# Performance work log

Measured on AMD Instinct MI355X. Metric: run time of the kernel, lower is better.

## Reference

```python
import jax, jax.numpy as jnp
import numpy as np
import math

B, T, C, H = 4, 2048, 1024, 4
D = C // H
SCALE = 1.0 / math.sqrt(D)
EPS = 1e-5

def _cln(x, w, b):
    # channel-first LayerNorm over C of (B, C, T)
    mu = jnp.mean(x, axis=1, keepdims=True)
    r = x - mu
    s = jnp.mean(r * r, axis=1, keepdims=True)
    return r / jnp.sqrt(s + EPS) * w + b

def _dwconv(x, w, b=None):
    # depthwise conv1d: x (B, C, T), w (C, 1, 3), stride 1, pad 1
    y = jax.lax.conv_general_dilated(x, w, (1,), [(1, 1)], dimension_numbers=('NCH', 'OIH', 'NCH'), feature_group_count=x.shape[1])
    if b is not None:
        y = y + b[None, :, None]
    return y

def _conv1x1(x, w, b):
    # pointwise conv: x (B, C, T), w (Cout, Cin), b (Cout,)
    return jnp.einsum('oc,bct->bot', w, x) + b[None, :, None]

def _forward(x, mask, norm1_w, norm1_b, qconv_w, kconv_w, vconv_w, qnorm_w, qnorm_b, knorm_w, knorm_b, vnorm_w, vnorm_b, q1_w, q1_b, k1_w, k1_b, v1_w, v1_b, proj_w, proj_b, norm2_w, norm2_b, lin1_w, lin1_b, tc_w, tc_b, lin2_w, lin2_b):
    xc = jnp.swapaxes(x, 1, 2)                      # (B, C, T)
    h = _cln(xc, norm1_w, norm1_b)
    mf = mask.astype(x.dtype)                       # (B, 1, T); stride 1 -> interpolate is identity
    q = _conv1x1(_cln(_dwconv(h, qconv_w) * mf, qnorm_w, qnorm_b), q1_w, q1_b)
    k = _conv1x1(_cln(_dwconv(h, kconv_w) * mf, knorm_w, knorm_b), k1_w, k1_b)
    v = _conv1x1(_cln(_dwconv(h, vconv_w) * mf, vnorm_w, vnorm_b), v1_w, v1_b)
    # (B, H, T, D)
    q = jnp.swapaxes(q.reshape(B, H, D, T), 2, 3)
    k = jnp.swapaxes(k.reshape(B, H, D, T), 2, 3)
    v = jnp.swapaxes(v.reshape(B, H, D, T), 2, 3)
    att = jnp.einsum('bhqd,bhkd->bhqk', q * SCALE, k)
    att = jnp.where(mask[:, :, None, :], att, -jnp.inf)
    att = jax.nn.softmax(att, axis=-1)
    out = jnp.einsum('bhqk,bhkd->bhqd', att, v * mf[:, :, :, None])
    out = jnp.swapaxes(out, 2, 3).reshape(B, C, T)
    out = _conv1x1(out, proj_w, proj_b) * mf        # qx_mask == mask for stride 1
    x = x + jnp.swapaxes(out, 1, 2)                 # residual, (B, T, C)
    # Local_cnn branch
    h2 = jnp.swapaxes(_cln(jnp.swapaxes(x, 1, 2), norm2_w, norm2_b), 1, 2)  # (B, T, C)
    y = h2 @ lin1_w.T + lin1_b
    y = jnp.swapaxes(_dwconv(jnp.swapaxes(y, 1, 2), tc_w, tc_b), 1, 2)
    y = jax.nn.gelu(y, approximate=False)
    y = y @ lin2_w.T + lin2_b
    return x + y

def setup_inputs():
    key = jax.random.key(0)
    ks = jax.random.split(key, 16)
    f32 = jnp.float32
    x = jax.random.normal(ks[0], (B, T, C), dtype=f32)
    lengths = jax.random.randint(ks[1], (B,), T // 2, T + 1)
    mask = jnp.arange(T)[None, None, :] < lengths[:, None, None]  # (B, 1, T) bool
    dw_std = math.sqrt(2.0 / 3.0)
    px_std = math.sqrt(2.0 / C)
    d = dict(x=x, mask=mask)
    d['norm1_w'] = jnp.ones((1, C, 1), f32); d['norm1_b'] = jnp.zeros((1, C, 1), f32)
    d['qconv_w'] = jax.random.normal(ks[2], (C, 1, 3), dtype=f32) * dw_std
    d['kconv_w'] = jax.random.normal(ks[3], (C, 1, 3), dtype=f32) * dw_std
    d['vconv_w'] = jax.random.normal(ks[4], (C, 1, 3), dtype=f32) * dw_std
    for nm in ['qnorm', 'knorm', 'vnorm']:
        d[nm + '_w'] = jnp.ones((1, C, 1), f32); d[nm + '_b'] = jnp.zeros((1, C, 1), f32)
    d['q1_w'] = jax.random.normal(ks[5], (C, C), dtype=f32) * px_std; d['q1_b'] = jnp.zeros((C,), f32)
    d['k1_w'] = jax.random.normal(ks[6], (C, C), dtype=f32) * px_std; d['k1_b'] = jnp.zeros((C,), f32)
    d['v1_w'] = jax.random.normal(ks[7], (C, C), dtype=f32) * px_std; d['v1_b'] = jnp.zeros((C,), f32)
    d['proj_w'] = jax.random.normal(ks[8], (C, C), dtype=f32) * px_std; d['proj_b'] = jnp.zeros((C,), f32)
    d['norm2_w'] = jnp.ones((1, C, 1), f32); d['norm2_b'] = jnp.zeros((1, C, 1), f32)
    d['lin1_w'] = jax.random.normal(ks[9], (C, C), dtype=f32) * 0.02; d['lin1_b'] = jnp.zeros((C,), f32)
    d['tc_w'] = jax.random.normal(ks[10], (C, 1, 3), dtype=f32) * dw_std; d['tc_b'] = jnp.zeros((C,), f32)
    d['lin2_w'] = jax.random.normal(ks[11], (C, C), dtype=f32) * 0.02; d['lin2_b'] = jnp.zeros((C,), f32)
    return d

def reference(x, mask, norm1_w, norm1_b, qconv_w, kconv_w, vconv_w, qnorm_w, qnorm_b, knorm_w, knorm_b, vnorm_w, vnorm_b, q1_w, q1_b, k1_w, k1_b, v1_w, v1_b, proj_w, proj_b, norm2_w, norm2_b, lin1_w, lin1_b, tc_w, tc_b, lin2_w, lin2_b):
    return _forward(x, mask, norm1_w, norm1_b, qconv_w, kconv_w, vconv_w, qnorm_w, qnorm_b, knorm_w, knorm_b, vnorm_w, vnorm_b, q1_w, q1_b, k1_w, k1_b, v1_w, v1_b, proj_w, proj_b, norm2_w, norm2_b, lin1_w, lin1_b, tc_w, tc_b, lin2_w, lin2_b)
```

## Files before the change

### kernel.cpp

```cpp
#include <hip/hip_runtime.h>

#define BB 4
#define TT 2048
#define CC 1024
#define HH 4
#define DD 256
#define MM (BB*TT)

#define EPSV 1e-5f
#define NEGBIG (-1e30f)
#define SCALEV 0.0625f

typedef unsigned short u16;
typedef unsigned int   u32;
typedef __bf16 bf16x8 __attribute__((ext_vector_type(8)));
typedef float  f32x4  __attribute__((ext_vector_type(4)));
typedef float  f32x16 __attribute__((ext_vector_type(16)));

typedef u32 __attribute__((address_space(1))) gu32;
typedef u32 __attribute__((address_space(3))) lu32;

__device__ __forceinline__ u16 f2bf(float f){
  u32 u = __builtin_bit_cast(u32, f);
  u32 r = (u + 0x7fffu + ((u >> 16) & 1u)) >> 16;
  return (u16)r;
}
__device__ __forceinline__ float bf2f(u16 h){
  u32 u = ((u32)h) << 16;
  return __builtin_bit_cast(float, u);
}
__device__ __forceinline__ void gload_lds16(const u16* g, u16* l){
  __builtin_amdgcn_global_load_lds((const gu32*)g, (lu32*)l, 16, 0, 0);
}
__device__ __forceinline__ u32 cvtpk_bf16(float lo, float hi){
  u32 r;
  asm("v_cvt_pk_bf16_f32 %0, %1, %2" : "=v"(r) : "v"(lo), "v"(hi));
  return r;
}

__global__ __launch_bounds__(256) void conv_w_kernel(
    const float* __restrict__ w0, const float* __restrict__ w1, const float* __restrict__ w2,
    const float* __restrict__ w3, const float* __restrict__ w4, const float* __restrict__ w5,
    u16* __restrict__ o0, u16* __restrict__ o1, u16* __restrict__ o2,
    u16* __restrict__ o3, u16* __restrict__ o4, u16* __restrict__ o5){
  const int i = (blockIdx.x * 256 + threadIdx.x) * 4;
  const float* wsrc[6] = {w0,w1,w2,w3,w4,w5};
  u16* odst[6] = {o0,o1,o2,o3,o4,o5};
#pragma unroll
  for (int k = 0; k < 6; ++k){
    float4 v = *(const float4*)(wsrc[k] + i);
    ushort4 p; p.x=f2bf(v.x); p.y=f2bf(v.y); p.z=f2bf(v.z); p.w=f2bf(v.w);
    *(ushort4*)(odst[k] + i) = p;
  }
}

template<int OUTBF>
__global__ __launch_bounds__(256) void ln_rows(const float* __restrict__ x,
    const float* __restrict__ g, const float* __restrict__ be, void* __restrict__ out){
  const int row = blockIdx.x, tid = threadIdx.x;
  const float4 v = ((const float4*)(x + (size_t)row * CC))[tid];
  float s  = v.x + v.y + v.z + v.w;
  float ss = v.x*v.x + v.y*v.y + v.z*v.z + v.w*v.w;
  __shared__ float sb[8];
#pragma unroll
  for (int o = 1; o < 64; o <<= 1){ s += __shfl_xor(s, o); ss += __shfl_xor(ss, o); }
  const int wid = tid >> 6, lane = tid & 63;
  if (lane == 0){ sb[wid] = s; sb[4 + wid] = ss; }
  __syncthreads();
  s  = sb[0] + sb[1] + sb[2] + sb[3];
  ss = sb[4] + sb[5] + sb[6] + sb[7];
  const float mu = s * (1.0f / CC);
  const float rstd = rsqrtf(ss * (1.0f / CC) - mu * mu + EPSV);
  const float4 gg = ((const float4*)g)[tid];
  const float4 bb = ((const float4*)be)[tid];
  const float r0 = (v.x - mu) * rstd * gg.x + bb.x;
  const float r1 = (v.y - mu) * rstd * gg.y + bb.y;
  const float r2 = (v.z - mu) * rstd * gg.z + bb.z;
  const float r3 = (v.w - mu) * rstd * gg.w + bb.w;
  if (OUTBF){
    ushort4 p; p.x=f2bf(r0); p.y=f2bf(r1); p.z=f2bf(r2); p.w=f2bf(r3);
    *(ushort4*)((u16*)out + (size_t)row * CC + tid * 4) = p;
  } else {
    ((float4*)((float*)out + (size_t)row * CC))[tid] = make_float4(r0, r1, r2, r3);
  }
}

__global__ __launch_bounds__(256) void qkv_pre(const u16* __restrict__ h,
    const int* __restrict__ mask,
    const float* __restrict__ qw, const float* __restrict__ kw, const float* __restrict__ vw,
    const float* __restrict__ qg, const float* __restrict__ qb2,
    const float* __restrict__ kg, const float* __restrict__ kb2,
    const float* __restrict__ vg, const float* __restrict__ vb2,
    u16* __restrict__ qn, u16* __restrict__ kn, u16* __restrict__ vn){
  const int row = blockIdx.x, tid = threadIdx.x;
  const int t = row & (TT - 1);
  const float mf = mask[row] ? 1.f : 0.f;
  ushort4 z4; z4.x = z4.y = z4.z = z4.w = 0;
  const ushort4 x0 = ((const ushort4*)(h + (size_t)row * CC))[tid];
  const ushort4 xm = (t > 0)      ? ((const ushort4*)(h + (size_t)(row - 1) * CC))[tid] : z4;
  const ushort4 xp = (t < TT - 1) ? ((const ushort4*)(h + (size_t)(row + 1) * CC))[tid] : z4;
  const int c = tid * 4;
  const float am[4] = {bf2f(xm.x), bf2f(xm.y), bf2f(xm.z), bf2f(xm.w)};
  const float a0[4] = {bf2f(x0.x), bf2f(x0.y), bf2f(x0.z), bf2f(x0.w)};
  const float ap[4] = {bf2f(xp.x), bf2f(xp.y), bf2f(xp.z), bf2f(xp.w)};
  float yq[4], yk[4], yv[4];
  float sq=0.f, ssq=0.f, sk=0.f, ssk=0.f, sv=0.f, ssv=0.f;
#pragma unroll
  for (int i = 0; i < 4; ++i){
    const float* qwp = qw + (c + i) * 3;
    const float* kwp = kw + (c + i) * 3;
    const float* vwp = vw + (c + i) * 3;
    const float q_ = (am[i]*qwp[0] + a0[i]*qwp[1] + ap[i]*qwp[2]) * mf;
    const float k_ = (am[i]*kwp[0] + a0[i]*kwp[1] + ap[i]*kwp[2]) * mf;
    const float v_ = (am[i]*vwp[0] + a0[i]*vwp[1] + ap[i]*vwp[2]) * mf;
    yq[i]=q_; yk[i]=k_; yv[i]=v_;
    sq+=q_; ssq+=q_*q_; sk+=k_; ssk+=k_*k_; sv+=v_; ssv+=v_*v_;
  }
  __shared__ float sb[24];
#pragma unroll
  for (int o = 1; o < 64; o <<= 1){
    sq += __shfl_xor(sq, o); ssq += __shfl_xor(ssq, o);
    sk += __shfl_xor(sk, o); ssk += __shfl_xor(ssk, o);
    sv += __shfl_xor(sv, o); ssv += __shfl_xor(ssv, o);
  }
  const int wid = tid >> 6, lane = tid & 63;
  if (lane == 0){
    sb[wid]=sq; sb[4+wid]=ssq; sb[8+wid]=sk; sb[12+wid]=ssk; sb[16+wid]=sv; sb[20+wid]=ssv;
  }
  __syncthreads();
  sq  = sb[0]+sb[1]+sb[2]+sb[3];    ssq = sb[4]+sb[5]+sb[6]+sb[7];
  sk  = sb[8]+sb[9]+sb[10]+sb[11];  ssk = sb[12]+sb[13]+sb[14]+sb[15];
  sv  = sb[16]+sb[17]+sb[18]+sb[19];ssv = sb[20]+sb[21]+sb[22]+sb[23];
  {
    const float mu = sq * (1.f/CC), rstd = rsqrtf(ssq*(1.f/CC) - mu*mu + EPSV);
    ushort4 p;
    p.x = f2bf((yq[0]-mu)*rstd*qg[c+0] + qb2[c+0]);
    p.y = f2bf((yq[1]-mu)*rstd*qg[c+1] + qb2[c+1]);
    p.z = f2bf((yq[2]-mu)*rstd*qg[c+2] + qb2[c+2]);
    p.w = f2bf((yq[3]-mu)*rstd*qg[c+3] + qb2[c+3]);
    *(ushort4*)(qn + (size_t)row * CC + c) = p;
  }
  {
    const float mu = sk * (1.f/CC), rstd = rsqrtf(ssk*(1.f/CC) - mu*mu + EPSV);
    ushort4 p;
    p.x = f2bf((yk[0]-mu)*rstd*kg[c+0] + kb2[c+0]);
    p.y = f2bf((yk[1]-mu)*rstd*kg[c+1] + kb2[c+1]);
    p.z = f2bf((yk[2]-mu)*rstd*kg[c+2] + kb2[c+2]);
    p.w = f2bf((yk[3]-mu)*rstd*kg[c+3] + kb2[c+3]);
    *(ushort4*)(kn + (size_t)row * CC + c) = p;
  }
  {
    const float mu = sv * (1.f/CC), rstd = rsqrtf(ssv*(1.f/CC) - mu*mu + EPSV);
    ushort4 p;
    p.x = f2bf((yv[0]-mu)*rstd*vg[c+0] + vb2[c+0]);
    p.y = f2bf((yv[1]-mu)*rstd*vg[c+1] + vb2[c+1]);
    p.z = f2bf((yv[2]-mu)*rstd*vg[c+2] + vb2[c+2]);
    p.w = f2bf((yv[3]-mu)*rstd*vg[c+3] + vb2[c+3]);
    *(ushort4*)(vn + (size_t)row * CC + c) = p;
  }
}

__device__ __forceinline__ void gemm_core(const u16* __restrict__ A, const u16* __restrict__ Bw,
    u16* As, u16* Bs, f32x4 acc[4][4], int bm, int bn, int tid){
  const int lane = tid & 63, wid = tid >> 6;
  const int wr = wid >> 1, wc = wid & 1;
  const int la = lane & 15, lg = lane >> 4;
  const int srow = tid >> 3;
  const int schunk = (tid & 7) ^ (srow & 7);
  const u16* gA = A  + (size_t)(bm * 128 + srow) * CC + schunk * 8;
  const u16* gB = Bw + (size_t)(bn * 128 + srow) * CC + schunk * 8;
  u16* dA = As + tid * 8;
  u16* dB = Bs + tid * 8;
  const int swz = (la & 7) << 4;
  for (int kt = 0; kt < CC / 64; ++kt){
#pragma unroll
    for (int i = 0; i < 4; ++i){
      gload_lds16(gA + (size_t)(i * 32) * CC + kt * 64, dA + i * 2048);
      gload_lds16(gB + (size_t)(i * 32) * CC + kt * 64, dB + i * 2048);
    }
    __syncthreads();
#pragma unroll
    for (int kk = 0; kk < 2; ++kk){
      bf16x8 af[4], bf[4];
      const int co = (kk * 64 + lg * 16) ^ swz;
#pragma unroll
      for (int mi = 0; mi < 4; ++mi)
        af[mi] = *(const bf16x8*)((const char*)As + (wr * 64 + mi * 16 + la) * 128 + co);
#pragma unroll
      for (int ni = 0; ni < 4; ++ni)
        bf[ni] = *(const bf16x8*)((const char*)Bs + (wc * 64 + ni * 16 + la) * 128 + co);
#pragma unroll
      for (int mi = 0; mi < 4; ++mi)
#pragma unroll
        for (int ni = 0; ni < 4; ++ni)
          acc[mi][ni] = __builtin_amdgcn_mfma_f32_16x16x32_bf16(af[mi], bf[ni], acc[mi][ni], 0, 0, 0);
    }
    __syncthreads();
  }
}

template<int MODE>
__global__ __launch_bounds__(256, 3) void gemm_bt(
    const u16* __restrict__ A, const u16* __restrict__ Bw,
    const float* __restrict__ bias, void* __restrict__ out,
    const float* __restrict__ resid, const int* __restrict__ mask){
  __shared__ __align__(16) u16 As[128 * 64];
  __shared__ __align__(16) u16 Bs[128 * 64];
  const int tid = threadIdx.x, lane = tid & 63, wid = tid >> 6;
  const int wr = wid >> 1, wc = wid & 1;
  const int bm = blockIdx.x, bn = blockIdx.y;
  f32x4 acc[4][4];
#pragma unroll
  for (int i = 0; i < 4; ++i)
#pragma unroll
    for (int j = 0; j < 4; ++j) acc[i][j] = (f32x4){0.f, 0.f, 0.f, 0.f};
  gemm_core(A, Bw, As, Bs, acc, bm, bn, tid);
  const int la = lane & 15, lg = lane >> 4;
#pragma unroll
  for (int mi = 0; mi < 4; ++mi){
    const int mb = bm * 128 + wr * 64 + mi * 16 + lg * 4;
#pragma unroll
    for (int ni = 0; ni < 4; ++ni){
      const int n = bn * 128 + wc * 64 + ni * 16 + la;
      const float bz = bias[n];
      if (MODE == 0){
        u16* o = (u16*)out;
#pragma unroll
        for (int j = 0; j < 4; ++j) o[(size_t)(mb + j) * CC + n] = f2bf(acc[mi][ni][j] + bz);
      } else if (MODE == 1){
        float* o = (float*)out;
#pragma unroll
        for (int j = 0; j < 4; ++j){
          const int m = mb + j;
          const float mf = mask[m] ? 1.f : 0.f;
          o[(size_t)m * CC + n] = (acc[mi][ni][j] + bz) * mf + resid[(size_t)m * CC + n];
        }
      } else {
        float* o = (float*)out;
#pragma unroll
        for (int j = 0; j < 4; ++j){
          const int m = mb + j;
          o[(size_t)m * CC + n] = acc[mi][ni][j] + bz + resid[(size_t)m * CC + n];
        }
      }
    }
  }
}

__global__ __launch_bounds__(256, 3) void gemm_qkv(
    const u16* __restrict__ qn, const u16* __restrict__ kn, const u16* __restrict__ vn,
    const u16* __restrict__ wq, const u16* __restrict__ wk, const u16* __restrict__ wv,
    const float* __restrict__ qb, const float* __restrict__ kb, const float* __restrict__ vb,
    u16* __restrict__ Qb, u16* __restrict__ Kb, u16* __restrict__ Vtb){
  __shared__ __align__(16) u16 As[128 * 64];
  __shared__ __align__(16) u16 Bs[128 * 64];
  const int z = blockIdx.z;
  const u16* A  = (z == 0) ? qn : (z == 1) ? kn : vn;
  const u16* Bw = (z == 0) ? wq : (z == 1) ? wk : wv;
  const float* bias = (z == 0) ? qb : (z == 1) ? kb : vb;
  const int tid = threadIdx.x, lane = tid & 63, wid = tid >> 6;
  const int wr = wid >> 1, wc = wid & 1;
  const int bm = blockIdx.x, bn = blockIdx.y;
  f32x4 acc[4][4];
#pragma unroll
  for (int i = 0; i < 4; ++i)
#pragma unroll
    for (int j = 0; j < 4; ++j) acc[i][j] = (f32x4){0.f, 0.f, 0.f, 0.f};
  gemm_core(A, Bw, As, Bs, acc, bm, bn, tid);
  const int la = lane & 15, lg = lane >> 4;
#pragma unroll
  for (int mi = 0; mi < 4; ++mi){
    const int mb = bm * 128 + wr * 64 + mi * 16 + lg * 4;
#pragma unroll
    for (int ni = 0; ni < 4; ++ni){
      const int n = bn * 128 + wc * 64 + ni * 16 + la;
      const float bz = bias[n];
      if (z < 2){
        u16* o = z ? Kb : Qb;
#pragma unroll
        for (int j = 0; j < 4; ++j) o[(size_t)(mb + j) * CC + n] = f2bf(acc[mi][ni][j] + bz);
      } else {
        const int bq = mb >> 11, tq = mb & (TT - 1);
        const int hq = n >> 8, dq = n & 255;
        ushort4 p;
        p.x = f2bf(acc[mi][ni][0] + bz); p.y = f2bf(acc[mi][ni][1] + bz);
        p.z = f2bf(acc[mi][ni][2] + bz); p.w = f2bf(acc[mi][ni][3] + bz);
        *(ushort4*)&Vtb[(size_t)((bq * HH + hq) * DD + dq) * TT + tq] = p;
      }
    }
  }
}

__global__ __launch_bounds__(256, 2) void flash_attn(
    const u16* __restrict__ Q, const u16* __restrict__ Kg,
    const u16* __restrict__ Vt, const int* __restrict__ mask,
    u16* __restrict__ Os0, u16* __restrict__ Os1, float2* __restrict__ stats){
  __shared__ __align__(16) u16 Ks[32 * 256];
  __shared__ __align__(16) u16 Vs[256 * 32];
  const int Dn = blockIdx.x;
  const int xcd = Dn & 7, rest = Dn >> 3;
  const int bh = xcd * 2 + (rest >> 5);
  const int sub = rest & 31;
  const int qt = sub >> 1, sp = sub & 1;
  const int b = bh >> 2, h2 = bh & 3;
  const int tid = threadIdx.x, lane = tid & 63, wid = tid >> 6;
  const int l31 = lane & 31, hi = lane >> 5;

  const int* mrow = mask + b * TT;
  int len = 1024;
  {
    unsigned long long bal = __ballot(mrow[1024 + lane * 16] != 0);
    int ones = __popcll(bal);
    if (ones > 0){
      int lo = 1024 + (ones - 1) * 16;
      unsigned long long bal2 = __ballot(mrow[lo + (lane & 15)] != 0);
      len = lo + __popcll(bal2 & 0xFFFFull);
    }
  }
  const int nkt = (len + 31) >> 5;
  const int hk = (nkt + 1) >> 1;
  const int t0 = sp ? hk : 0, t1 = sp ? nkt : hk;

  const int q0 = qt * 128 + wid * 32;
  bf16x8 qf[16];
  const u16* qrow = Q + (size_t)(b * TT + q0 + l31) * CC + h2 * DD + hi * 8;
#pragma unroll
  for (int kd = 0; kd < 16; ++kd) qf[kd] = *(const bf16x8*)(qrow + kd * 16);

  f32x16 acc[8];
#pragma unroll
  for (int i = 0; i < 8; ++i)
#pragma unroll
    for (int r = 0; r < 16; ++r) acc[i][r] = 0.f;
  float mrun = NEGBIG, lrun = 0.f;

  const int krow = tid >> 5;
  const int kc = (tid & 31) ^ (krow & 7);
  const u16* ksrc = Kg + (size_t)(b * TT + krow) * CC + h2 * DD + kc * 8;
  const int vc = (tid & 3) ^ ((tid >> 3) & 3);
  const u16* vsrcb = Vt + (size_t)(bh * DD + (tid >> 2)) * TT + vc * 8;

#define STAGE_K(KT) { _Pragma("unroll") \
  for (int i = 0; i < 4; ++i) \
    gload_lds16(ksrc + (size_t)((KT) * 32 + i * 8) * CC, Ks + i * 2048 + tid * 8); }
#define STAGE_V(KT) { _Pragma("unroll") \
  for (int i = 0; i < 4; ++i) \
    gload_lds16(vsrcb + (size_t)(i * 64) * TT + (KT) * 32, Vs + i * 2048 + tid * 8); }

  STAGE_K(t0); STAGE_V(t0);
  __syncthreads();

  const char* KsB = (const char*)Ks;
  const char* VsB = (const char*)Vs;
  const int swk = (l31 & 7) << 4;
  const int swv = ((l31 >> 1) & 3) << 4;
  const float sc2 = SCALEV * 1.44269504f;

  for (int kt = t0; kt < t1; ++kt){
    f32x16 s;
#pragma unroll
    for (int r = 0; r < 16; ++r) s[r] = 0.f;
#pragma unroll
    for (int kd = 0; kd < 16; ++kd){
      bf16x8 kf = *(const bf16x8*)(KsB + l31 * 512 + ((kd * 32 + hi * 16) ^ swk));
      s = __builtin_amdgcn_mfma_f32_32x32x16_bf16(kf, qf[kd], s, 0, 0, 0);
    }
    if (kt * 32 + 32 <= len){
      s *= sc2;
    } else {
#pragma unroll
      for (int r = 0; r < 16; ++r){
        const int k = kt * 32 + (r & 3) + 8 * (r >> 2) + 4 * hi;
        s[r] = (k < len) ? s[r] * sc2 : NEGBIG;
      }
    }
    float tm = s[0];
#pragma unroll
    for (int r = 1; r < 16; ++r) tm = fmaxf(tm, s[r]);
    tm = fmaxf(tm, __shfl_xor(tm, 32));
    if (!__all(tm <= mrun + 12.0f)){
      const float mn = fmaxf(mrun, tm);
      const float al = __builtin_exp2f(mrun - mn);
      mrun = mn; lrun *= al;
#pragma unroll
      for (int i = 0; i < 8; ++i) acc[i] *= al;
    }
    float p[16];
    float ts = 0.f;
#pragma unroll
    for (int r = 0; r < 16; ++r){ p[r] = __builtin_exp2f(s[r] - mrun); ts += p[r]; }
    ts += __shfl_xor(ts, 32);
    lrun += ts;
    u32 w0 = cvtpk_bf16(p[0],  p[1]),  w1 = cvtpk_bf16(p[2],  p[3]);
    u32 w2 = cvtpk_bf16(p[4],  p[5]),  w3 = cvtpk_bf16(p[6],  p[7]);
    u32 w4 = cvtpk_bf16(p[8],  p[9]),  w5 = cvtpk_bf16(p[10], p[11]);
    u32 w6 = cvtpk_bf16(p[12], p[13]), w7 = cvtpk_bf16(p[14], p[15]);
    asm("v_permlane32_swap_b32 %0, %1" : "+v"(w0), "+v"(w2));
    asm("v_permlane32_swap_b32 %0, %1" : "+v"(w1), "+v"(w3));
    asm("v_permlane32_swap_b32 %0, %1" : "+v"(w4), "+v"(w6));
    asm("v_permlane32_swap_b32 %0, %1" : "+v"(w5), "+v"(w7));
    u32 pb0u[4] = {w0, w1, w2, w3};
    u32 pb1u[4] = {w4, w5, w6, w7};
    bf16x8 pb0 = __builtin_bit_cast(bf16x8, *(uint4*)pb0u);
    bf16x8 pb1 = __builtin_bit_cast(bf16x8, *(uint4*)pb1u);
    __syncthreads();
    if (kt + 1 < t1) STAGE_K(kt + 1);
#pragma unroll
    for (int dt = 0; dt < 8; ++dt){
      const char* vr = VsB + (dt * 32 + l31) * 64;
      bf16x8 vf0 = *(const bf16x8*)(vr + ((hi * 16) ^ swv));
      acc[dt] = __builtin_amdgcn_mfma_f32_32x32x16_bf16(vf0, pb0, acc[dt], 0, 0, 0);
      bf16x8 vf1 = *(const bf16x8*)(vr + ((32 + hi * 16) ^ swv));
      acc[dt] = __builtin_amdgcn_mfma_f32_32x32x16_bf16(vf1, pb1, acc[dt], 0, 0, 0);
    }
    __syncthreads();
    if (kt + 1 < t1) STAGE_V(kt + 1);
  }
  u16* Os = sp ? Os1 : Os0;
  u16* orow = Os + (size_t)(b * TT + q0 + l31) * CC + h2 * DD + hi * 4;
#pragma unroll
  for (int dt = 0; dt < 8; ++dt)
#pragma unroll
    for (int rg = 0; rg < 4; ++rg){
      ushort4 pk;
      pk.x = f2bf(acc[dt][rg * 4 + 0]); pk.y = f2bf(acc[dt][rg * 4 + 1]);
      pk.z = f2bf(acc[dt][rg * 4 + 2]); pk.w = f2bf(acc[dt][rg * 4 + 3]);
      *(ushort4*)(orow + dt * 32 + rg * 8) = pk;
    }
  if (lane < 32)
    stats[(size_t)((sp * 16 + bh) << 11) + q0 + l31] = make_float2(mrun, lrun);
#undef STAGE_K
#undef STAGE_V
}

__global__ __launch_bounds__(256) void attn_combine(
    const u16* __restrict__ Os0, const u16* __restrict__ Os1,
    const float2* __restrict__ stats, u16* __restrict__ AO){
  const int row = blockIdx.x, tid = threadIdx.x;
  const int b = row >> 11, q = row & (TT - 1);
  const int h2 = tid >> 6;
  const int bh = b * HH + h2;
  const float2 sA = stats[(size_t)(bh << 11) + q];
  const float2 sB = stats[(size_t)((16 + bh) << 11) + q];
  const float m = fmaxf(sA.x, sB.x);
  const float eA = __builtin_exp2f(sA.x - m), eB = __builtin_exp2f(sB.x - m);
  const float l = sA.y * eA + sB.y * eB;
  const float fA = eA / l, fB = eB / l;
  const size_t off = (size_t)row * CC + tid * 4;
  const ushort4 a = *(const ushort4*)(Os0 + off);
  const ushort4 c = *(const ushort4*)(Os1 + off);
  ushort4 o;
  o.x = f2bf(bf2f(a.x) * fA + bf2f(c.x) * fB);
  o.y = f2bf(bf2f(a.y) * fA + bf2f(c.y) * fB);
  o.z = f2bf(bf2f(a.z) * fA + bf2f(c.z) * fB);
  o.w = f2bf(bf2f(a.w) * fA + bf2f(c.w) * fB);
  *(ushort4*)(AO + off) = o;
}

__global__ __launch_bounds__(256) void tc_gelu(const u16* __restrict__ y2,
    const float* __restrict__ w, const float* __restrict__ bias, u16* __restrict__ y3){
  const int row = blockIdx.x, tid = threadIdx.x;
  const int t = row & (TT - 1);
  const int c = tid * 4;
  ushort4 z4; z4.x = z4.y = z4.z = z4.w = 0;
  const ushort4 u0 = *(const ushort4*)(y2 + (size_t)row * CC + c);
  const ushort4 um = (t > 0)      ? *(const ushort4*)(y2 + (size_t)(row - 1) * CC + c) : z4;
  const ushort4 up = (t < TT - 1) ? *(const ushort4*)(y2 + (size_t)(row + 1) * CC + c) : z4;
  const float am[4] = {bf2f(um.x), bf2f(um.y), bf2f(um.z), bf2f(um.w)};
  const float a0[4] = {bf2f(u0.x), bf2f(u0.y), bf2f(u0.z), bf2f(u0.w)};
  const float ap[4] = {bf2f(up.x), bf2f(up.y), bf2f(up.z), bf2f(up.w)};
  u16 pv[4];
#pragma unroll
  for (int i = 0; i < 4; ++i){
    const float* wp = w + (c + i) * 3;
    const float yv = am[i] * wp[0] + a0[i] * wp[1] + ap[i] * wp[2] + bias[c + i];
    const float ge = 0.5f * yv * (1.f + erff(yv * 0.7071067811865475f));
    pv[i] = f2bf(ge);
  }
  ushort4 p; p.x = pv[0]; p.y = pv[1]; p.z = pv[2]; p.w = pv[3];
  *(ushort4*)(y3 + (size_t)row * CC + c) = p;
}

extern "C" void kernel_launch(void* const* d_in, const int* in_sizes, int n_in,
                              void* d_out, int out_size, void* d_ws, size_t ws_size,
                              hipStream_t stream){
  const float* x     = (const float*)d_in[0];
  const int*   mask  = (const int*)d_in[1];
  const float* n1g   = (const float*)d_in[2];
  const float* n1b   = (const float*)d_in[3];
  const float* qconv = (const float*)d_in[4];
  const float* kconv = (const float*)d_in[5];
  const float* vconv = (const float*)d_in[6];
  const float* qg    = (const float*)d_in[7];
  const float* qbe   = (const float*)d_in[8];
  const float* kg    = (const float*)d_in[9];
  const float* kbe   = (const float*)d_in[10];
  const float* vg    = (const float*)d_in[11];
  const float* vbe   = (const float*)d_in[12];
  const float* q1w   = (const float*)d_in[13];
  const float* q1b   = (const float*)d_in[14];
  const float* k1w   = (const float*)d_in[15];
  const float* k1b   = (const float*)d_in[16];
  const float* v1w   = (const float*)d_in[17];
  const float* v1b   = (const float*)d_in[18];
  const float* pw    = (const float*)d_in[19];
  const float* pb    = (const float*)d_in[20];
  const float* n2g   = (const float*)d_in[21];
  const float* n2b   = (const float*)d_in[22];
  const float* l1w   = (const float*)d_in[23];
  const float* l1b   = (const float*)d_in[24];
  const float* tcw   = (const float*)d_in[25];
  const float* tcb   = (const float*)d_in[26];
  const float* l2w   = (const float*)d_in[27];
  const float* l2b   = (const float*)d_in[28];
  (void)in_sizes; (void)n_in; (void)out_size; (void)ws_size;

  char* ws = (char*)d_ws;
  const size_t MB = (size_t)1 << 20;
  u16* wq  = (u16*)(ws + 0 * MB);
  u16* wk  = (u16*)(ws + 2 * MB);
  u16* wv  = (u16*)(ws + 4 * MB);
  u16* wp2 = (u16*)(ws + 6 * MB);
  u16* wl1 = (u16*)(ws + 8 * MB);
  u16* wl2 = (u16*)(ws + 10 * MB);
  u16* hbuf = (u16*)(ws + 12 * MB);
  float* x2 = (float*)(ws + 12 * MB);
  u16* qn  = (u16*)(ws + 44 * MB);
  u16* kn  = (u16*)(ws + 60 * MB);
  u16* vn  = (u16*)(ws + 76 * MB);
  u16* Qb  = (u16*)(ws + 92 * MB);
  u16* Kb  = (u16*)(ws + 108 * MB);
  u16* Vtb = (u16*)(ws + 124 * MB);
  float2* stats = (float2*)(ws + 140 * MB);
  u16* AO  = qn;
  u16* Os0 = kn;
  u16* Os1 = vn;
  u16* y1  = kn;
  u16* y2  = vn;
  u16* y3  = Qb;

  conv_w_kernel<<<1024, 256, 0, stream>>>(q1w, k1w, v1w, pw, l1w, l2w, wq, wk, wv, wp2, wl1, wl2);
  ln_rows<1><<<MM, 256, 0, stream>>>(x, n1g, n1b, hbuf);
  qkv_pre<<<MM, 256, 0, stream>>>(hbuf, mask, qconv, kconv, vconv,
                                  qg, qbe, kg, kbe, vg, vbe, qn, kn, vn);
  gemm_qkv<<<dim3(64, 8, 3), 256, 0, stream>>>(qn, kn, vn, wq, wk, wv, q1b, k1b, v1b, Qb, Kb, Vtb);
  flash_attn<<<512, 256, 0, stream>>>(Qb, Kb, Vtb, mask, Os0, Os1, stats);
  attn_combine<<<MM, 256, 0, stream>>>(Os0, Os1, stats, AO);
  gemm_bt<1><<<dim3(64, 8), 256, 0, stream>>>(AO, wp2, pb, x2, x, mask);
  ln_rows<1><<<MM, 256, 0, stream>>>(x2, n2g, n2b, y1);
  gemm_bt<0><<<dim3(64, 8), 256, 0, stream>>>(y1, wl1, l1b, y2, nullptr, nullptr);
  tc_gelu<<<MM, 256, 0, stream>>>(y2, tcw, tcb, y3);
  gemm_bt<2><<<dim3(64, 8), 256, 0, stream>>>(y3, wl2, l2b, (float*)d_out, x2, nullptr);
}
```

Baseline: 330.9 us.

## Double-buffer GEMM LDS tiles and store the mid-block residual in bf16

The shared GEMM core now uses two LDS buffers per operand. The global-to-LDS copy for the next K tile is issued before the MFMAs on the current tile, which hides load latency behind compute. This doubles LDS per block, so the occupancy hint for gemm_bt and gemm_qkv drops from 3 to 2 blocks. Separately, the post-attention residual x2 is written as bf16 instead of fp32, with a new bf16-input LayerNorm kernel and a bf16 residual read in the final GEMM, which cuts memory traffic but adds rounding error to the residual path.

```diff
diff --git a/kernel.cpp b/kernel.cpp
--- a/kernel.cpp
+++ b/kernel.cpp
@@ -54,9 +54,8 @@
   }
 }
 
-template<int OUTBF>
 __global__ __launch_bounds__(256) void ln_rows(const float* __restrict__ x,
-    const float* __restrict__ g, const float* __restrict__ be, void* __restrict__ out){
+    const float* __restrict__ g, const float* __restrict__ be, u16* __restrict__ out){
   const int row = blockIdx.x, tid = threadIdx.x;
   const float4 v = ((const float4*)(x + (size_t)row * CC))[tid];
   float s  = v.x + v.y + v.z + v.w;
@@ -73,16 +72,39 @@
   const float rstd = rsqrtf(ss * (1.0f / CC) - mu * mu + EPSV);
   const float4 gg = ((const float4*)g)[tid];
   const float4 bb = ((const float4*)be)[tid];
-  const float r0 = (v.x - mu) * rstd * gg.x + bb.x;
-  const float r1 = (v.y - mu) * rstd * gg.y + bb.y;
-  const float r2 = (v.z - mu) * rstd * gg.z + bb.z;
-  const float r3 = (v.w - mu) * rstd * gg.w + bb.w;
-  if (OUTBF){
-    ushort4 p; p.x=f2bf(r0); p.y=f2bf(r1); p.z=f2bf(r2); p.w=f2bf(r3);
-    *(ushort4*)((u16*)out + (size_t)row * CC + tid * 4) = p;
-  } else {
-    ((float4*)((float*)out + (size_t)row * CC))[tid] = make_float4(r0, r1, r2, r3);
-  }
+  ushort4 p;
+  p.x = f2bf((v.x - mu) * rstd * gg.x + bb.x);
+  p.y = f2bf((v.y - mu) * rstd * gg.y + bb.y);
+  p.z = f2bf((v.z - mu) * rstd * gg.z + bb.z);
+  p.w = f2bf((v.w - mu) * rstd * gg.w + bb.w);
+  *(ushort4*)(out + (size_t)row * CC + tid * 4) = p;
+}
+
+__global__ __launch_bounds__(256) void ln_rows_b2b(const u16* __restrict__ x,
+    const float* __restrict__ g, const float* __restrict__ be, u16* __restrict__ out){
+  const int row = blockIdx.x, tid = threadIdx.x;
+  const ushort4 u = ((const ushort4*)(x + (size_t)row * CC))[tid];
+  const float v0 = bf2f(u.x), v1 = bf2f(u.y), v2 = bf2f(u.z), v3 = bf2f(u.w);
+  float s  = v0 + v1 + v2 + v3;
+  float ss = v0*v0 + v1*v1 + v2*v2 + v3*v3;
+  __shared__ float sb[8];
+#pragma unroll
+  for (int o = 1; o < 64; o <<= 1){ s += __shfl_xor(s, o); ss += __shfl_xor(ss, o); }
+  const int wid = tid >> 6, lane = tid & 63;
+  if (lane == 0){ sb[wid] = s; sb[4 + wid] = ss; }
+  __syncthreads();
+  s  = sb[0] + sb[1] + sb[2] + sb[3];
+  ss = sb[4] + sb[5] + sb[6] + sb[7];
+  const float mu = s * (1.0f / CC);
+  const float rstd = rsqrtf(ss * (1.0f / CC) - mu * mu + EPSV);
+  const float4 gg = ((const float4*)g)[tid];
+  const float4 bb = ((const float4*)be)[tid];
+  ushort4 p;
+  p.x = f2bf((v0 - mu) * rstd * gg.x + bb.x);
+  p.y = f2bf((v1 - mu) * rstd * gg.y + bb.y);
+  p.z = f2bf((v2 - mu) * rstd * gg.z + bb.z);
+  p.w = f2bf((v3 - mu) * rstd * gg.w + bb.w);
+  *(ushort4*)(out + (size_t)row * CC + tid * 4) = p;
 }
 
 __global__ __launch_bounds__(256) void qkv_pre(const u16* __restrict__ h,
@@ -169,26 +191,33 @@
   const int schunk = (tid & 7) ^ (srow & 7);
   const u16* gA = A  + (size_t)(bm * 128 + srow) * CC + schunk * 8;
   const u16* gB = Bw + (size_t)(bn * 128 + srow) * CC + schunk * 8;
-  u16* dA = As + tid * 8;
-  u16* dB = Bs + tid * 8;
   const int swz = (la & 7) << 4;
+  auto stage = [&](int KT, int BUF){
+    u16* dA = As + BUF * 8192 + tid * 8;
+    u16* dB = Bs + BUF * 8192 + tid * 8;
+#pragma unroll
+    for (int i = 0; i < 4; ++i){
+      gload_lds16(gA + (size_t)(i * 32) * CC + KT * 64, dA + i * 2048);
+      gload_lds16(gB + (size_t)(i * 32) * CC + KT * 64, dB + i * 2048);
+    }
+  };
+  stage(0, 0);
+  __syncthreads();
   for (int kt = 0; kt < CC / 64; ++kt){
-#pragma unroll
-    for (int i = 0; i < 4; ++i){
-      gload_lds16(gA + (size_t)(i * 32) * CC + kt * 64, dA + i * 2048);
-      gload_lds16(gB + (size_t)(i * 32) * CC + kt * 64, dB + i * 2048);
-    }
-    __syncthreads();
+    const int cur = kt & 1;
+    if (kt + 1 < CC / 64) stage(kt + 1, cur ^ 1);
+    const char* AsB = (const char*)(As + cur * 8192);
+    const char* BsB = (const char*)(Bs + cur * 8192);
 #pragma unroll
     for (int kk = 0; kk < 2; ++kk){
       bf16x8 af[4], bf[4];
       const int co = (kk * 64 + lg * 16) ^ swz;
 #pragma unroll
       for (int mi = 0; mi < 4; ++mi)
-        af[mi] = *(const bf16x8*)((const char*)As + (wr * 64 + mi * 16 + la) * 128 + co);
+        af[mi] = *(const bf16x8*)(AsB + (wr * 64 + mi * 16 + la) * 128 + co);
 #pragma unroll
       for (int ni = 0; ni < 4; ++ni)
-        bf[ni] = *(const bf16x8*)((const char*)Bs + (wc * 64 + ni * 16 + la) * 128 + co);
+        bf[ni] = *(const bf16x8*)(BsB + (wc * 64 + ni * 16 + la) * 128 + co);
 #pragma unroll
       for (int mi = 0; mi < 4; ++mi)
 #pragma unroll
@@ -200,12 +229,12 @@
 }
 
 template<int MODE>
-__global__ __launch_bounds__(256, 3) void gemm_bt(
+__global__ __launch_bounds__(256, 2) void gemm_bt(
     const u16* __restrict__ A, const u16* __restrict__ Bw,
     const float* __restrict__ bias, void* __restrict__ out,
-    const float* __restrict__ resid, const int* __restrict__ mask){
-  __shared__ __align__(16) u16 As[128 * 64];
-  __shared__ __align__(16) u16 Bs[128 * 64];
+    const void* __restrict__ resid, const int* __restrict__ mask){
+  __shared__ __align__(16) u16 As[2 * 8192];
+  __shared__ __align__(16) u16 Bs[2 * 8192];
   const int tid = threadIdx.x, lane = tid & 63, wid = tid >> 6;
   const int wr = wid >> 1, wc = wid & 1;
   const int bm = blockIdx.x, bn = blockIdx.y;
@@ -228,32 +257,34 @@
 #pragma unroll
         for (int j = 0; j < 4; ++j) o[(size_t)(mb + j) * CC + n] = f2bf(acc[mi][ni][j] + bz);
       } else if (MODE == 1){
-        float* o = (float*)out;
+        u16* o = (u16*)out;
+        const float* r = (const float*)resid;
 #pragma unroll
         for (int j = 0; j < 4; ++j){
           const int m = mb + j;
           const float mf = mask[m] ? 1.f : 0.f;
-          o[(size_t)m * CC + n] = (acc[mi][ni][j] + bz) * mf + resid[(size_t)m * CC + n];
+          o[(size_t)m * CC + n] = f2bf((acc[mi][ni][j] + bz) * mf + r[(size_t)m * CC + n]);
         }
       } else {
         float* o = (float*)out;
+        const u16* r = (const u16*)resid;
 #pragma unroll
         for (int j = 0; j < 4; ++j){
           const int m = mb + j;
-          o[(size_t)m * CC + n] = acc[mi][ni][j] + bz + resid[(size_t)m * CC + n];
+          o[(size_t)m * CC + n] = acc[mi][ni][j] + bz + bf2f(r[(size_t)m * CC + n]);
         }
       }
     }
   }
 }
 
-__global__ __launch_bounds__(256, 3) void gemm_qkv(
+__global__ __launch_bounds__(256, 2) void gemm_qkv(
     const u16* __restrict__ qn, const u16* __restrict__ kn, const u16* __restrict__ vn,
     const u16* __restrict__ wq, const u16* __restrict__ wk, const u16* __restrict__ wv,
     const float* __restrict__ qb, const float* __restrict__ kb, const float* __restrict__ vb,
     u16* __restrict__ Qb, u16* __restrict__ Kb, u16* __restrict__ Vtb){
-  __shared__ __align__(16) u16 As[128 * 64];
-  __shared__ __align__(16) u16 Bs[128 * 64];
+  __shared__ __align__(16) u16 As[2 * 8192];
+  __shared__ __align__(16) u16 Bs[2 * 8192];
   const int z = blockIdx.z;
   const u16* A  = (z == 0) ? qn : (z == 1) ? kn : vn;
   const u16* Bw = (z == 0) ? wq : (z == 1) ? wk : wv;
@@ -524,7 +555,7 @@
   u16* wl1 = (u16*)(ws + 8 * MB);
   u16* wl2 = (u16*)(ws + 10 * MB);
   u16* hbuf = (u16*)(ws + 12 * MB);
-  float* x2 = (float*)(ws + 12 * MB);
+  u16* x2b  = (u16*)(ws + 12 * MB);
   u16* qn  = (u16*)(ws + 44 * MB);
   u16* kn  = (u16*)(ws + 60 * MB);
   u16* vn  = (u16*)(ws + 76 * MB);
@@ -540,15 +571,15 @@
   u16* y3  = Qb;
 
   conv_w_kernel<<<1024, 256, 0, stream>>>(q1w, k1w, v1w, pw, l1w, l2w, wq, wk, wv, wp2, wl1, wl2);
-  ln_rows<1><<<MM, 256, 0, stream>>>(x, n1g, n1b, hbuf);
+  ln_rows<<<MM, 256, 0, stream>>>(x, n1g, n1b, hbuf);
   qkv_pre<<<MM, 256, 0, stream>>>(hbuf, mask, qconv, kconv, vconv,
                                   qg, qbe, kg, kbe, vg, vbe, qn, kn, vn);
   gemm_qkv<<<dim3(64, 8, 3), 256, 0, stream>>>(qn, kn, vn, wq, wk, wv, q1b, k1b, v1b, Qb, Kb, Vtb);
   flash_attn<<<512, 256, 0, stream>>>(Qb, Kb, Vtb, mask, Os0, Os1, stats);
   attn_combine<<<MM, 256, 0, stream>>>(Os0, Os1, stats, AO);
-  gemm_bt<1><<<dim3(64, 8), 256, 0, stream>>>(AO, wp2, pb, x2, x, mask);
-  ln_rows<1><<<MM, 256, 0, stream>>>(x2, n2g, n2b, y1);
+  gemm_bt<1><<<dim3(64, 8), 256, 0, stream>>>(AO, wp2, pb, x2b, x, mask);
+  ln_rows_b2b<<<MM, 256, 0, stream>>>(x2b, n2g, n2b, y1);
   gemm_bt<0><<<dim3(64, 8), 256, 0, stream>>>(y1, wl1, l1b, y2, nullptr, nullptr);
   tc_gelu<<<MM, 256, 0, stream>>>(y2, tcw, tcb, y3);
-  gemm_bt<2><<<dim3(64, 8), 256, 0, stream>>>(y3, wl2, l2b, (float*)d_out, x2, nullptr);
-}
+  gemm_bt<2><<<dim3(64, 8), 256, 0, stream>>>(y3, wl2, l2b, (float*)d_out, x2b, nullptr);
+}
```

After: 317.1 us. 1.04x faster.
